# Performance work log

Hardware: AMD Instinct MI355X
Metric: run time of the kernel (lower is better)

Reference implementation:

```python
import jax, jax.numpy as jnp
import numpy as np

B, C, V, L = 64, 32, 1024, 12
ORDER = 2


def setup_inputs() -> dict:
    key = jax.random.key(0)
    ks = jax.random.split(key, 6)
    x = jax.random.normal(ks[0], (B, C, V, L), dtype=jnp.float32)
    A1 = jax.random.uniform(ks[1], (V, V), dtype=jnp.float32)
    A2 = jax.random.uniform(ks[2], (V, V), dtype=jnp.float32)
    nodevec1 = jax.random.normal(ks[3], (V, 10), dtype=jnp.float32)
    nodevec2 = jax.random.normal(ks[4], (10, V), dtype=jnp.float32)
    c_cat = (ORDER * 3 + 1) * C  # 7*C = 224, matches gcn: (order*support_len+1)*c_in
    W_mlp = jax.random.normal(ks[5], (C, c_cat), dtype=jnp.float32) * 0.05
    b_mlp = jnp.zeros((C,), dtype=jnp.float32)
    return {"x": x, "A1": A1, "A2": A2, "nodevec1": nodevec1,
            "nodevec2": nodevec2, "W_mlp": W_mlp, "b_mlp": b_mlp}


def reference(x, A1, A2, nodevec1, nodevec2, W_mlp, b_mlp):
    # adaptive adjacency: softmax(relu(E1 @ E2), dim=1)  (graph-wavenet style)
    adp = jax.nn.softmax(jax.nn.relu(nodevec1 @ nodevec2), axis=1)  # [V, V]
    supports = (A1, A2, adp)
    # gcn.forward: multi-hop diffusion via nconv einsum, order=2
    out = [x]
    for a in supports:
        x1 = jnp.einsum('ncvl,vw->ncwl', x, a)   # hop 1
        out.append(x1)
        x2 = jnp.einsum('ncvl,vw->ncwl', x1, a)  # hop 2
        out.append(x2)
    h = jnp.concatenate(out, axis=1)             # [B, 7C, V, L]
    # linear: 1x1 Conv2d over channel dim (dropout is identity in eval)
    h = jnp.einsum('ncvl,oc->novl', h, W_mlp) + b_mlp[None, :, None, None]
    return h
```

## Files before the change

### kernel.cpp

```cpp
#include <hip/hip_runtime.h>
#include <hip/hip_bf16.h>


typedef __attribute__((ext_vector_type(8))) short short8;
typedef __attribute__((ext_vector_type(4))) float floatx4;

#define V_DIM 1024
#define L_DIM 12
#define B_DIM 64
#define C_DIM 32

__global__ __launch_bounds__(128) void adp_kernel(
    const float* __restrict__ nv1, const float* __restrict__ nv2,
    float* __restrict__ adp) {
  const int v = blockIdx.x, tid = threadIdx.x;
  float n1[10];
#pragma unroll
  for (int i = 0; i < 10; ++i) n1[i] = nv1[v * 10 + i];
  __shared__ float red[128];
  float e[8];
  float lmax = -1e30f;
#pragma unroll
  for (int j = 0; j < 8; ++j) {
    int w = tid + j * 128;
    float s = 0.f;
#pragma unroll
    for (int i = 0; i < 10; ++i) s += n1[i] * nv2[i * V_DIM + w];
    s = fmaxf(s, 0.f);
    e[j] = s;
    lmax = fmaxf(lmax, s);
  }
  red[tid] = lmax; __syncthreads();
  for (int s = 64; s > 0; s >>= 1) {
    if (tid < s) red[tid] = fmaxf(red[tid], red[tid + s]);
    __syncthreads();
  }
  float mx = red[0]; __syncthreads();
  float lsum = 0.f;
#pragma unroll
  for (int j = 0; j < 8; ++j) { e[j] = __expf(e[j] - mx); lsum += e[j]; }
  red[tid] = lsum; __syncthreads();
  for (int s = 64; s > 0; s >>= 1) {
    if (tid < s) red[tid] += red[tid + s];
    __syncthreads();
  }
  float inv = 1.f / red[0];
#pragma unroll
  for (int j = 0; j < 8; ++j) adp[(size_t)v * V_DIM + tid + j * 128] = e[j] * inv;
}

__global__ __launch_bounds__(256) void cast_transpose(
    const float* __restrict__ A1, const float* __restrict__ A2,
    const float* __restrict__ adp, __hip_bfloat16* __restrict__ As,
    __hip_bfloat16* __restrict__ BtCat) {
  const int z = blockIdx.z;
  const float* src = (z == 0) ? A1 : (z == 1) ? A2 : adp;
  __hip_bfloat16* sdst = As + (size_t)z * V_DIM * V_DIM;
  __hip_bfloat16* tdst = BtCat + (size_t)(2 * z) * V_DIM * V_DIM;
  __shared__ float tile[64][65];
  const int v0 = blockIdx.y * 64, w0 = blockIdx.x * 64;
  const int tc = threadIdx.x & 15, tr = threadIdx.x >> 4;
#pragma unroll
  for (int i = 0; i < 4; ++i) {
    int r = tr + i * 16;
    float4 val = *(const float4*)(src + (size_t)(v0 + r) * V_DIM + w0 + tc * 4);
    tile[r][tc * 4 + 0] = val.x; tile[r][tc * 4 + 1] = val.y;
    tile[r][tc * 4 + 2] = val.z; tile[r][tc * 4 + 3] = val.w;
    __hip_bfloat16* sp = sdst + (size_t)(v0 + r) * V_DIM + w0 + tc * 4;
    sp[0] = __float2bfloat16(val.x); sp[1] = __float2bfloat16(val.y);
    sp[2] = __float2bfloat16(val.z); sp[3] = __float2bfloat16(val.w);
  }
  __syncthreads();
#pragma unroll
  for (int i = 0; i < 4; ++i) {
    int r = tr + i * 16;
    __hip_bfloat16* tp = tdst + (size_t)(w0 + r) * V_DIM + v0 + tc * 4;
#pragma unroll
    for (int j = 0; j < 4; ++j) tp[j] = __float2bfloat16(tile[tc * 4 + j][r]);
  }
}

__global__ __launch_bounds__(256) void transpose_x_k(
    const float* __restrict__ x, __hip_bfloat16* __restrict__ xT) {
  const int bc = blockIdx.x;
  const int b = bc >> 5, c = bc & 31;
  __shared__ __align__(16) __hip_bfloat16 tile[V_DIM * L_DIM];
  const float4* src = (const float4*)(x + (size_t)bc * (V_DIM * L_DIM));
#pragma unroll
  for (int i = 0; i < 12; ++i) {
    int idx = threadIdx.x + i * 256;
    float4 v = src[idx];
    int e = idx * 4;
    tile[e + 0] = __float2bfloat16(v.x); tile[e + 1] = __float2bfloat16(v.y);
    tile[e + 2] = __float2bfloat16(v.z); tile[e + 3] = __float2bfloat16(v.w);
  }
  __syncthreads();
  for (int l = 0; l < L_DIM; ++l) {
    __hip_bfloat16* dst = xT + ((size_t)(b * L_DIM + l) * C_DIM + c) * V_DIM;
    for (int v = threadIdx.x; v < V_DIM; v += 256) dst[v] = tile[v * L_DIM + l];
  }
}

__device__ __forceinline__ void gll16(const __hip_bfloat16* g, __hip_bfloat16* l) {
  __builtin_amdgcn_global_load_lds(
      (const __attribute__((address_space(1))) void*)g,
      (__attribute__((address_space(3))) void*)l, 16, 0, 0);
}

template <int MODE>
__global__ __launch_bounds__(256) void gemm_bt(
    const __hip_bfloat16* __restrict__ Abase,
    const __hip_bfloat16* __restrict__ Btbase,
    __hip_bfloat16* __restrict__ Cbase, int M, int N, int K,
    long long aStride, long long bStride, long long cStride) {
  const __hip_bfloat16* A = Abase + (size_t)blockIdx.z * aStride;
  const __hip_bfloat16* Bt = Btbase + (size_t)blockIdx.z * bStride;
  __hip_bfloat16* C = Cbase + (size_t)blockIdx.z * cStride;
  __shared__ __align__(16) __hip_bfloat16 lA[128 * 64];
  __shared__ __align__(16) __hip_bfloat16 lB[128 * 64];
  const int tid = threadIdx.x;
  const int wv = tid >> 6, lane = tid & 63;
  const int wm = wv >> 1, wn = wv & 1;
  const int m0 = blockIdx.y * 128, n0 = blockIdx.x * 128;
  const int lrow = lane >> 3, lcol = lane & 7;
  const int gcol = lcol ^ (lrow & 7);
  const int fr = lane & 15, quad = lane >> 4;
  const int sw = fr & 7;

  floatx4 acc[4][4];
#pragma unroll
  for (int i = 0; i < 4; ++i)
#pragma unroll
    for (int j = 0; j < 4; ++j) acc[i][j] = (floatx4){0.f, 0.f, 0.f, 0.f};

  for (int kt = 0; kt < K; kt += 64) {
    __syncthreads();
#pragma unroll
    for (int i = 0; i < 4; ++i) {
      int r0 = (wv * 4 + i) * 8;
      gll16(A + (size_t)(m0 + r0 + lrow) * K + kt + gcol * 8, &lA[r0 * 64]);
      gll16(Bt + (size_t)(n0 + r0 + lrow) * K + kt + gcol * 8, &lB[r0 * 64]);
    }
    __syncthreads();
#pragma unroll
    for (int ks = 0; ks < 2; ++ks) {
      const int chunk = (ks * 4 + quad) ^ sw;
      short8 af[4], bfr[4];
#pragma unroll
      for (int t = 0; t < 4; ++t) {
        af[t] = *(const short8*)&lA[(wm * 64 + t * 16 + fr) * 64 + chunk * 8];
        bfr[t] = *(const short8*)&lB[(wn * 64 + t * 16 + fr) * 64 + chunk * 8];
      }
#pragma unroll
      for (int i = 0; i < 4; ++i)
#pragma unroll
        for (int j = 0; j < 4; ++j)
          acc[i][j] = __builtin_amdgcn_mfma_f32_16x16x32_bf16(af[i], bfr[j], acc[i][j], 0, 0, 0);
    }
  }
#pragma unroll
  for (int i = 0; i < 4; ++i) {
#pragma unroll
    for (int j = 0; j < 4; ++j) {
      int mb = m0 + wm * 64 + i * 16 + quad * 4;
      int n = n0 + wn * 64 + j * 16 + fr;
#pragma unroll
      for (int r = 0; r < 4; ++r) {
        int m = mb + r;
        float val = acc[i][j][r];
        size_t idx;
        if (MODE == 0) {
          idx = (size_t)m * N + n;
        } else {
          int c = m & 31, bl = m >> 5, k = n >> 10, w = n & 1023;
          idx = (((size_t)bl * 6 + k) * 32 + c) * 1024 + w;
        }
        C[idx] = __float2bfloat16(val);
      }
    }
  }
}

__global__ __launch_bounds__(512, 2) void gemm256(
    const __hip_bfloat16* __restrict__ A,
    const __hip_bfloat16* __restrict__ Bt,
    __hip_bfloat16* __restrict__ C) {
  constexpr int K = 1024;
  constexpr int NH = K / 32;
  __shared__ __align__(16) __hip_bfloat16 sA[4][8192];
  __shared__ __align__(16) __hip_bfloat16 sB[4][8192];
  const int tid = threadIdx.x;
  const int wv = tid >> 6, lane = tid & 63;
  const int wm = wv >> 2, wn = wv & 3;
  const int fr = lane & 15, quad = lane >> 4;
  const int rslot = (quad ^ ((fr >> 1) & 3)) << 3;
  const int aoff = (wm * 128 + fr) * 32 + rslot;
  const int boff = (wn * 64 + fr) * 32 + rslot;
  const int m0 = blockIdx.y * 256, n0 = blockIdx.x * 256;
  const int srow = wv * 32 + (lane >> 2);
  const int gch = ((lane & 3) ^ ((lane >> 3) & 3)) << 3;
  const __hip_bfloat16* Ag = A + (size_t)(m0 + srow) * K + gch;
  const __hip_bfloat16* Bg = Bt + (size_t)(n0 + srow) * K + gch;
  const int sbase = (wv * 32) * 32;

  floatx4 acc[8][4];
#pragma unroll
  for (int i = 0; i < 8; ++i)
#pragma unroll
    for (int j = 0; j < 4; ++j) acc[i][j] = (floatx4){0.f, 0.f, 0.f, 0.f};

#pragma unroll
  for (int hp = 0; hp < 3; ++hp) {
    gll16(Ag + hp * 32, &sA[hp][sbase]);
    gll16(Ag + (size_t)16 * K + hp * 32, &sA[hp][sbase + 512]);
    gll16(Bg + hp * 32, &sB[hp][sbase]);
    gll16(Bg + (size_t)16 * K + hp * 32, &sB[hp][sbase + 512]);
  }
  asm volatile("s_waitcnt vmcnt(8)" ::: "memory");
  __builtin_amdgcn_s_barrier();

  for (int h = 0; h < NH; ++h) {
    const int u = h & 3;
    short8 af[4], bf[4];
#pragma unroll
    for (int j = 0; j < 4; ++j) bf[j] = *(const short8*)&sB[u][boff + j * 512];
#pragma unroll
    for (int i = 0; i < 4; ++i) af[i] = *(const short8*)&sA[u][aoff + i * 512];
    if (h + 3 < NH) {
      const int h3 = h + 3, u3 = h3 & 3;
      gll16(Ag + h3 * 32, &sA[u3][sbase]);
      gll16(Ag + (size_t)16 * K + h3 * 32, &sA[u3][sbase + 512]);
    }
    __builtin_amdgcn_s_barrier();
    __builtin_amdgcn_s_setprio(1);
#pragma unroll
    for (int i = 0; i < 4; ++i)
#pragma unroll
      for (int j = 0; j < 4; ++j)
        acc[i][j] = __builtin_amdgcn_mfma_f32_16x16x32_bf16(af[i], bf[j], acc[i][j], 0, 0, 0);
    __builtin_amdgcn_s_setprio(0);
    __builtin_amdgcn_s_barrier();
#pragma unroll
    for (int i = 0; i < 4; ++i) af[i] = *(const short8*)&sA[u][aoff + (4 + i) * 512];
    if (h + 3 < NH) {
      const int h3 = h + 3, u3 = h3 & 3;
      gll16(Bg + h3 * 32, &sB[u3][sbase]);
      gll16(Bg + (size_t)16 * K + h3 * 32, &sB[u3][sbase + 512]);
    }
    __builtin_amdgcn_s_barrier();
    __builtin_amdgcn_s_setprio(1);
#pragma unroll
    for (int i = 0; i < 4; ++i)
#pragma unroll
      for (int j = 0; j < 4; ++j)
        acc[4 + i][j] = __builtin_amdgcn_mfma_f32_16x16x32_bf16(af[i], bf[j], acc[4 + i][j], 0, 0, 0);
    __builtin_amdgcn_s_setprio(0);
    if (h < NH - 3) {
      asm volatile("s_waitcnt vmcnt(8)" ::: "memory");
    } else if (h == NH - 3) {
      asm volatile("s_waitcnt vmcnt(4)" ::: "memory");
    } else if (h == NH - 2) {
      asm volatile("s_waitcnt vmcnt(0)" ::: "memory");
    }
    __builtin_amdgcn_s_barrier();
  }

#pragma unroll
  for (int i = 0; i < 8; ++i) {
#pragma unroll
    for (int j = 0; j < 4; ++j) {
      int mb = m0 + wm * 128 + i * 16 + quad * 4;
      int n = n0 + wn * 64 + j * 16 + fr;
      int k = n >> 10, w = n & 1023;
#pragma unroll
      for (int r = 0; r < 4; ++r) {
        int m = mb + r;
        int c = m & 31, bl = m >> 5;
        size_t idx = (((size_t)bl * 6 + k) * 32 + c) * 1024 + w;
        C[idx] = __float2bfloat16(acc[i][j][r]);
      }
    }
  }
}

__global__ __launch_bounds__(256) void mix_kernel(
    const __hip_bfloat16* __restrict__ R, const __hip_bfloat16* __restrict__ xT,
    const float* __restrict__ W, const float* __restrict__ bias,
    float* __restrict__ out) {
  const int b = blockIdx.y, wt = blockIdx.x;
  const int tid = threadIdx.x;
  __shared__ __align__(16) __hip_bfloat16 tile[L_DIM * C_DIM * 64];
  __shared__ float Wl[7 * 32 * 32];
  for (int i = tid; i < 7168; i += 256) {
    int o = i / 224, cc = i - o * 224;
    Wl[cc * 32 + o] = W[i];
  }
  float acc[3][32];
#pragma unroll
  for (int pt = 0; pt < 3; ++pt)
#pragma unroll
    for (int o = 0; o < 32; ++o) acc[pt][o] = bias[o];
  int wloc[3], ll[3];
#pragma unroll
  for (int pt = 0; pt < 3; ++pt) {
    int wl = tid + pt * 256;
    wloc[pt] = wl / 12;
    ll[pt] = wl - wloc[pt] * 12;
  }
  const int w0 = wt * 64;
  for (int k = 0; k < 7; ++k) {
    __syncthreads();
    const __hip_bfloat16* srcp = (k < 6) ? R : xT;
    const int rps = (k < 6) ? 192 : 32;
    const int ko = (k < 6) ? k * 32 : 0;
#pragma unroll
    for (int i = 0; i < 24; ++i) {
      int q = tid + i * 256;
      int rr = q >> 4, ci = q & 15;
      int l = rr >> 5, c = rr & 31;
      size_t rowg = (size_t)(b * L_DIM + l) * rps + ko + c;
      *(ushort4*)&tile[rr * 64 + ci * 4] =
          *(const ushort4*)&srcp[rowg * V_DIM + w0 + ci * 4];
    }
    __syncthreads();
    const float* Wp = &Wl[((k < 6) ? (k + 1) : 0) * 1024];
    const int base0 = ll[0] * 2048 + wloc[0];
    const int base1 = ll[1] * 2048 + wloc[1];
    const int base2 = ll[2] * 2048 + wloc[2];
#pragma unroll 8
    for (int c = 0; c < 32; ++c) {
      float v0 = __bfloat162float(tile[base0 + c * 64]);
      float v1 = __bfloat162float(tile[base1 + c * 64]);
      float v2 = __bfloat162float(tile[base2 + c * 64]);
#pragma unroll
      for (int o = 0; o < 32; ++o) {
        float wv = Wp[c * 32 + o];
        acc[0][o] += wv * v0;
        acc[1][o] += wv * v1;
        acc[2][o] += wv * v2;
      }
    }
  }
  const size_t obase = (size_t)b * (32 * V_DIM * L_DIM) + (size_t)w0 * L_DIM;
#pragma unroll
  for (int o = 0; o < 32; ++o) {
    size_t base = obase + (size_t)o * (V_DIM * L_DIM);
    out[base + tid] = acc[0][o];
    out[base + tid + 256] = acc[1][o];
    out[base + tid + 512] = acc[2][o];
  }
}

extern "C" void kernel_launch(void* const* d_in, const int* in_sizes, int n_in,
                              void* d_out, int out_size, void* d_ws,
                              size_t ws_size, hipStream_t stream) {
  const float* x = (const float*)d_in[0];
  const float* A1 = (const float*)d_in[1];
  const float* A2 = (const float*)d_in[2];
  const float* nv1 = (const float*)d_in[3];
  const float* nv2 = (const float*)d_in[4];
  const float* W = (const float*)d_in[5];
  const float* bias = (const float*)d_in[6];
  float* out = (float*)d_out;

  char* ws = (char*)d_ws;
  __hip_bfloat16* R = (__hip_bfloat16*)(ws + 0);
  __hip_bfloat16* xT = (__hip_bfloat16*)(ws + 301989888ull);
  __hip_bfloat16* BtCat = (__hip_bfloat16*)(ws + 352321536ull);
  __hip_bfloat16* As = (__hip_bfloat16*)(ws + 364904448ull);
  float* adp = (float*)(ws + 371195904ull);

  adp_kernel<<<dim3(1024), dim3(128), 0, stream>>>(nv1, nv2, adp);
  cast_transpose<<<dim3(16, 16, 3), dim3(256), 0, stream>>>(A1, A2, adp, As, BtCat);
  gemm_bt<0><<<dim3(8, 8, 3), dim3(256), 0, stream>>>(
      BtCat, As, BtCat + 1048576ull, 1024, 1024, 1024,
      2097152ll, 1048576ll, 2097152ll);
  transpose_x_k<<<dim3(2048), dim3(256), 0, stream>>>(x, xT);
  gemm256<<<dim3(24, 96), dim3(512), 0, stream>>>(xT, BtCat, R);
  mix_kernel<<<dim3(16, 64), dim3(256), 0, stream>>>(R, xT, W, bias, out);
}
```

Measured before the change: 766.9 us.

## Prefetch next K-step LDS fragments during second MFMA phase with ping-pong registers

Restructures the bf16 GEMM main loop so that the B fragments and first-half A fragments for the next K-step are read from LDS during the current step's second MFMA phase. Two register sets alternate across an unrolled-by-two loop. The vmcnt waits are tightened so the next stage is resident before it is read. This hides LDS read latency behind MFMA work, at the cost of more VGPRs and a possible hazard if NH is odd or the waits are wrong.

Result: no change. 765.6 us (-0.2%).

```diff
diff --git a/kernel.cpp b/kernel.cpp
--- a/kernel.cpp
+++ b/kernel.cpp
@@ -216,54 +216,72 @@
     gll16(Bg + hp * 32, &sB[hp][sbase]);
     gll16(Bg + (size_t)16 * K + hp * 32, &sB[hp][sbase + 512]);
   }
-  asm volatile("s_waitcnt vmcnt(8)" ::: "memory");
+  asm volatile("s_waitcnt vmcnt(4)" ::: "memory");
   __builtin_amdgcn_s_barrier();
 
-  for (int h = 0; h < NH; ++h) {
-    const int u = h & 3;
-    short8 af[4], bf[4];
-#pragma unroll
-    for (int j = 0; j < 4; ++j) bf[j] = *(const short8*)&sB[u][boff + j * 512];
-#pragma unroll
-    for (int i = 0; i < 4; ++i) af[i] = *(const short8*)&sA[u][aoff + i * 512];
-    if (h + 3 < NH) {
-      const int h3 = h + 3, u3 = h3 & 3;
-      gll16(Ag + h3 * 32, &sA[u3][sbase]);
-      gll16(Ag + (size_t)16 * K + h3 * 32, &sA[u3][sbase + 512]);
-    }
-    __builtin_amdgcn_s_barrier();
-    __builtin_amdgcn_s_setprio(1);
-#pragma unroll
-    for (int i = 0; i < 4; ++i)
-#pragma unroll
-      for (int j = 0; j < 4; ++j)
-        acc[i][j] = __builtin_amdgcn_mfma_f32_16x16x32_bf16(af[i], bf[j], acc[i][j], 0, 0, 0);
-    __builtin_amdgcn_s_setprio(0);
-    __builtin_amdgcn_s_barrier();
-#pragma unroll
-    for (int i = 0; i < 4; ++i) af[i] = *(const short8*)&sA[u][aoff + (4 + i) * 512];
-    if (h + 3 < NH) {
-      const int h3 = h + 3, u3 = h3 & 3;
-      gll16(Bg + h3 * 32, &sB[u3][sbase]);
-      gll16(Bg + (size_t)16 * K + h3 * 32, &sB[u3][sbase + 512]);
-    }
-    __builtin_amdgcn_s_barrier();
-    __builtin_amdgcn_s_setprio(1);
-#pragma unroll
-    for (int i = 0; i < 4; ++i)
-#pragma unroll
-      for (int j = 0; j < 4; ++j)
-        acc[4 + i][j] = __builtin_amdgcn_mfma_f32_16x16x32_bf16(af[i], bf[j], acc[4 + i][j], 0, 0, 0);
-    __builtin_amdgcn_s_setprio(0);
-    if (h < NH - 3) {
-      asm volatile("s_waitcnt vmcnt(8)" ::: "memory");
-    } else if (h == NH - 3) {
-      asm volatile("s_waitcnt vmcnt(4)" ::: "memory");
-    } else if (h == NH - 2) {
-      asm volatile("s_waitcnt vmcnt(0)" ::: "memory");
-    }
-    __builtin_amdgcn_s_barrier();
-  }
+  short8 bfA[4], af0A[4], bfB[4], af0B[4], af1[4];
+#pragma unroll
+  for (int j = 0; j < 4; ++j) bfA[j] = *(const short8*)&sB[0][boff + j * 512];
+#pragma unroll
+  for (int i = 0; i < 4; ++i) af0A[i] = *(const short8*)&sA[0][aoff + i * 512];
+
+#define P0(h, bfC, af0C)                                                     \
+  {                                                                          \
+    const int u_ = (h) & 3;                                                  \
+    _Pragma("unroll") for (int i = 0; i < 4; ++i)                            \
+        af1[i] = *(const short8*)&sA[u_][aoff + (4 + i) * 512];              \
+    if ((h) + 3 < NH) {                                                      \
+      const int u3_ = ((h) + 3) & 3;                                         \
+      gll16(Ag + ((h) + 3) * 32, &sA[u3_][sbase]);                           \
+      gll16(Ag + (size_t)16 * K + ((h) + 3) * 32, &sA[u3_][sbase + 512]);    \
+    }                                                                        \
+    __builtin_amdgcn_s_barrier();                                            \
+    __builtin_amdgcn_s_setprio(1);                                           \
+    _Pragma("unroll") for (int i = 0; i < 4; ++i)                            \
+        _Pragma("unroll") for (int j = 0; j < 4; ++j)                        \
+            acc[i][j] = __builtin_amdgcn_mfma_f32_16x16x32_bf16(             \
+                af0C[i], bfC[j], acc[i][j], 0, 0, 0);                        \
+    __builtin_amdgcn_s_setprio(0);                                           \
+    __builtin_amdgcn_s_barrier();                                            \
+  }
+
+#define P1(h, bfC, bfN, af0N)                                                \
+  {                                                                          \
+    if ((h) + 1 < NH) {                                                      \
+      const int un_ = ((h) + 1) & 3;                                         \
+      _Pragma("unroll") for (int j = 0; j < 4; ++j)                          \
+          bfN[j] = *(const short8*)&sB[un_][boff + j * 512];                 \
+      _Pragma("unroll") for (int i = 0; i < 4; ++i)                          \
+          af0N[i] = *(const short8*)&sA[un_][aoff + i * 512];                \
+    }                                                                        \
+    if ((h) + 3 < NH) {                                                      \
+      const int u3_ = ((h) + 3) & 3;                                         \
+      gll16(Bg + ((h) + 3) * 32, &sB[u3_][sbase]);                           \
+      gll16(Bg + (size_t)16 * K + ((h) + 3) * 32, &sB[u3_][sbase + 512]);    \
+    }                                                                        \
+    if ((h) < NH - 3) {                                                      \
+      asm volatile("s_waitcnt vmcnt(4)" ::: "memory");                       \
+    } else if ((h) == NH - 3) {                                              \
+      asm volatile("s_waitcnt vmcnt(0)" ::: "memory");                       \
+    }                                                                        \
+    __builtin_amdgcn_s_barrier();                                            \
+    __builtin_amdgcn_s_setprio(1);                                           \
+    _Pragma("unroll") for (int i = 0; i < 4; ++i)                            \
+        _Pragma("unroll") for (int j = 0; j < 4; ++j)                        \
+            acc[4 + i][j] = __builtin_amdgcn_mfma_f32_16x16x32_bf16(         \
+                af1[i], bfC[j], acc[4 + i][j], 0, 0, 0);                     \
+    __builtin_amdgcn_s_setprio(0);                                           \
+    __builtin_amdgcn_s_barrier();                                            \
+  }
+
+  for (int hh = 0; hh < NH; hh += 2) {
+    P0(hh, bfA, af0A)
+    P1(hh, bfA, bfB, af0B)
+    P0(hh + 1, bfB, af0B)
+    P1(hh + 1, bfB, bfA, af0A)
+  }
+#undef P0
+#undef P1
 
 #pragma unroll
   for (int i = 0; i < 8; ++i) {
```

## Shrink main GEMM tile to 256x128 with 4 waves and 3-stage pipeline

Applied to the files above, without the earlier changes.

Reworks the main bf16 GEMM from a 256x256 tile with 8 waves and a 4-buffer, 3-ahead prefetch into a 256x128 tile with 4 waves and a 3-buffer, 2-ahead prefetch. Each iteration now issues all 32 MFMAs after a single LDS read phase, replacing the two half-phases and cutting per-iteration barriers from three to one. This doubles the grid and lowers LDS per block, which can help occupancy and tail balance. The cost is less operand reuse per block (more global/L2 traffic for A) and shallower latency hiding.

After: 758.0 us. Within noise of the previous version (-1.2%).

```diff
diff --git a/kernel.cpp b/kernel.cpp
--- a/kernel.cpp
+++ b/kernel.cpp
@@ -181,27 +181,26 @@
   }
 }
 
-__global__ __launch_bounds__(512, 2) void gemm256(
+__global__ __launch_bounds__(256, 2) void gemm256(
     const __hip_bfloat16* __restrict__ A,
     const __hip_bfloat16* __restrict__ Bt,
     __hip_bfloat16* __restrict__ C) {
   constexpr int K = 1024;
   constexpr int NH = K / 32;
-  __shared__ __align__(16) __hip_bfloat16 sA[4][8192];
-  __shared__ __align__(16) __hip_bfloat16 sB[4][8192];
+  __shared__ __align__(16) __hip_bfloat16 sA[3][256 * 32];
+  __shared__ __align__(16) __hip_bfloat16 sB[3][128 * 32];
   const int tid = threadIdx.x;
   const int wv = tid >> 6, lane = tid & 63;
-  const int wm = wv >> 2, wn = wv & 3;
+  const int wm = wv >> 1, wn = wv & 1;
   const int fr = lane & 15, quad = lane >> 4;
   const int rslot = (quad ^ ((fr >> 1) & 3)) << 3;
   const int aoff = (wm * 128 + fr) * 32 + rslot;
   const int boff = (wn * 64 + fr) * 32 + rslot;
-  const int m0 = blockIdx.y * 256, n0 = blockIdx.x * 256;
-  const int srow = wv * 32 + (lane >> 2);
+  const int m0 = blockIdx.y * 256, n0 = blockIdx.x * 128;
   const int gch = ((lane & 3) ^ ((lane >> 3) & 3)) << 3;
-  const __hip_bfloat16* Ag = A + (size_t)(m0 + srow) * K + gch;
-  const __hip_bfloat16* Bg = Bt + (size_t)(n0 + srow) * K + gch;
-  const int sbase = (wv * 32) * 32;
+  const __hip_bfloat16* Ag = A + (size_t)(m0 + wv * 16 + (lane >> 2)) * K + gch;
+  const __hip_bfloat16* Bg = Bt + (size_t)(n0 + wv * 16 + (lane >> 2)) * K + gch;
+  const int sb = (wv * 16) * 32;
 
   floatx4 acc[8][4];
 #pragma unroll
@@ -209,61 +208,44 @@
 #pragma unroll
     for (int j = 0; j < 4; ++j) acc[i][j] = (floatx4){0.f, 0.f, 0.f, 0.f};
 
-#pragma unroll
-  for (int hp = 0; hp < 3; ++hp) {
-    gll16(Ag + hp * 32, &sA[hp][sbase]);
-    gll16(Ag + (size_t)16 * K + hp * 32, &sA[hp][sbase + 512]);
-    gll16(Bg + hp * 32, &sB[hp][sbase]);
-    gll16(Bg + (size_t)16 * K + hp * 32, &sB[hp][sbase + 512]);
-  }
-  asm volatile("s_waitcnt vmcnt(8)" ::: "memory");
+#define STAGE(hp, ur)                                                        \
+  {                                                                          \
+    _Pragma("unroll") for (int j = 0; j < 4; ++j)                            \
+        gll16(Ag + (size_t)(j * 64) * K + (hp) * 32, &sA[ur][sb + j * 2048]);\
+    _Pragma("unroll") for (int j = 0; j < 2; ++j)                            \
+        gll16(Bg + (size_t)(j * 64) * K + (hp) * 32, &sB[ur][sb + j * 2048]);\
+  }
+
+  STAGE(0, 0)
+  STAGE(1, 1)
+  asm volatile("s_waitcnt vmcnt(6)" ::: "memory");
   __builtin_amdgcn_s_barrier();
 
+  int u = 0, us = 2;
   for (int h = 0; h < NH; ++h) {
-    const int u = h & 3;
-    short8 af[4], bf[4];
+    short8 af[8], bf[4];
 #pragma unroll
     for (int j = 0; j < 4; ++j) bf[j] = *(const short8*)&sB[u][boff + j * 512];
 #pragma unroll
-    for (int i = 0; i < 4; ++i) af[i] = *(const short8*)&sA[u][aoff + i * 512];
-    if (h + 3 < NH) {
-      const int h3 = h + 3, u3 = h3 & 3;
-      gll16(Ag + h3 * 32, &sA[u3][sbase]);
-      gll16(Ag + (size_t)16 * K + h3 * 32, &sA[u3][sbase + 512]);
-    }
-    __builtin_amdgcn_s_barrier();
+    for (int i = 0; i < 8; ++i) af[i] = *(const short8*)&sA[u][aoff + i * 512];
+    if (h < NH - 2) STAGE(h + 2, us)
     __builtin_amdgcn_s_setprio(1);
 #pragma unroll
-    for (int i = 0; i < 4; ++i)
+    for (int i = 0; i < 8; ++i)
 #pragma unroll
       for (int j = 0; j < 4; ++j)
         acc[i][j] = __builtin_amdgcn_mfma_f32_16x16x32_bf16(af[i], bf[j], acc[i][j], 0, 0, 0);
     __builtin_amdgcn_s_setprio(0);
-    __builtin_amdgcn_s_barrier();
-#pragma unroll
-    for (int i = 0; i < 4; ++i) af[i] = *(const short8*)&sA[u][aoff + (4 + i) * 512];
-    if (h + 3 < NH) {
-      const int h3 = h + 3, u3 = h3 & 3;
-      gll16(Bg + h3 * 32, &sB[u3][sbase]);
-      gll16(Bg + (size_t)16 * K + h3 * 32, &sB[u3][sbase + 512]);
-    }
-    __builtin_amdgcn_s_barrier();
-    __builtin_amdgcn_s_setprio(1);
-#pragma unroll
-    for (int i = 0; i < 4; ++i)
-#pragma unroll
-      for (int j = 0; j < 4; ++j)
-        acc[4 + i][j] = __builtin_amdgcn_mfma_f32_16x16x32_bf16(af[i], bf[j], acc[4 + i][j], 0, 0, 0);
-    __builtin_amdgcn_s_setprio(0);
-    if (h < NH - 3) {
-      asm volatile("s_waitcnt vmcnt(8)" ::: "memory");
-    } else if (h == NH - 3) {
-      asm volatile("s_waitcnt vmcnt(4)" ::: "memory");
+    if (h < NH - 2) {
+      asm volatile("s_waitcnt vmcnt(6)" ::: "memory");
     } else if (h == NH - 2) {
       asm volatile("s_waitcnt vmcnt(0)" ::: "memory");
     }
     __builtin_amdgcn_s_barrier();
-  }
+    u = (u == 2) ? 0 : u + 1;
+    us = (us == 2) ? 0 : us + 1;
+  }
+#undef STAGE
 
 #pragma unroll
   for (int i = 0; i < 8; ++i) {
@@ -376,6 +358,6 @@
       BtCat, As, BtCat + 1048576ull, 1024, 1024, 1024,
       2097152ll, 1048576ll, 2097152ll);
   transpose_x_k<<<dim3(2048), dim3(256), 0, stream>>>(x, xT);
-  gemm256<<<dim3(24, 96), dim3(512), 0, stream>>>(xT, BtCat, R);
+  gemm256<<<dim3(48, 96), dim3(256), 0, stream>>>(xT, BtCat, R);
   mix_kernel<<<dim3(16, 64), dim3(256), 0, stream>>>(R, xT, W, bias, out);
 }
```
